# Kernel optimization log

Hardware: AMD Instinct MI355X
Metric: run time of the kernel (lower is better)

Reference implementation:

```python
import jax, jax.numpy as jnp
import numpy as np

LBDA = 0.5  # soft-min temperature, matches OTAM_cum_dist_v2 default


def setup_inputs() -> dict:
    key = jax.random.key(0)
    # frame distance scores (e.g. 1 - cosine similarity), in [0, 2]
    dists = jax.random.uniform(key, (200, 200, 32, 32), dtype=jnp.float32) * 2.0
    return {"dists": dists}


def _otam_cum_dist(dists, lbda=LBDA):
    """Faithful translation of OTAM_cum_dist_v2.

    dists: [Q, S, L, M] -> returns cum_dists[:, :, -1, -1] of shape [Q, S].
    The torch code pads the last dim by (1,1) with zeros, does a cumulative
    sum along row 0, and for each subsequent row a serial soft-min
    (-lbda * log(sum(exp(-x/lbda)))) recurrence along columns. Column 0 is
    never written and stays 0. Columns m==1 and m==Mp-1 include an extra
    diagonal/above term prev_row[m]; interior columns use only prev_row[m-1]
    and the running value cum[l, m-1].
    """
    Q, S, L, M = dists.shape
    Mp = M + 2
    # pad last dim by one zero on each side, move (L, Mp) to the front
    d = jnp.pad(dists, ((0, 0), (0, 0), (0, 0), (1, 1)))
    d = jnp.transpose(d, (2, 3, 0, 1))  # [L, Mp, Q, S]

    # row 0: cum[0, m] = cum[0, m-1] + d[0, m]; d[0,0]=0 so plain cumsum works
    row0 = jnp.cumsum(d[0], axis=0)  # [Mp, Q, S]

    m_idx = jnp.arange(1, Mp)
    mask3 = (m_idx == 1) | (m_idx == Mp - 1)  # columns with the 3-term soft-min

    def row_step(prev_row, d_row):
        # prev_row, d_row: [Mp, Q, S]
        def col_step(c, xs):
            d_m, p_m1, p_m, m3 = xs
            # soft-min: -lbda * log( exp(-p_m1/l) + exp(-c/l) [+ exp(-p_m/l)] )
            s = jnp.logaddexp(-p_m1 / lbda, -c / lbda)
            s = jnp.where(m3, jnp.logaddexp(s, -p_m / lbda), s)
            v = d_m - lbda * s
            return v, v

        xs = (d_row[1:], prev_row[:-1], prev_row[1:], mask3)
        _, vals = jax.lax.scan(col_step, jnp.zeros_like(d_row[0]), xs)
        new_row = jnp.concatenate([jnp.zeros_like(vals[:1]), vals], axis=0)
        return new_row, 0.0

    last_row, _ = jax.lax.scan(row_step, row0, d[1:])
    return last_row[-1]  # cum_dists[:, :, -1, -1] -> [Q, S]


def reference(dists):
    return _otam_cum_dist(dists, LBDA)
```

## Files before the change

kernel.cpp:

```cpp
#include <hip/hip_runtime.h>
#include <math.h>


constexpr int QS = 200 * 200;
constexpr int L = 32;
constexpr int M = 32;

__global__ __launch_bounds__(64) void otam_kernel(const float* __restrict__ dists,
                                                  float* __restrict__ out) {
    int p = blockIdx.x * blockDim.x + threadIdx.x;
    if (p >= QS) return;
    const float* dp = dists + (size_t)p * (L * M);

    float prev[34];
    float rowbuf[32];

    {
        const float4* r4 = (const float4*)dp;
#pragma unroll
        for (int i = 0; i < 8; ++i) {
            float4 v = r4[i];
            rowbuf[4 * i + 0] = v.x;
            rowbuf[4 * i + 1] = v.y;
            rowbuf[4 * i + 2] = v.z;
            rowbuf[4 * i + 3] = v.w;
        }
        float acc = 0.f;
        prev[0] = 0.f;
#pragma unroll
        for (int m = 1; m <= 32; ++m) {
            acc += rowbuf[m - 1];
            prev[m] = acc;
        }
        prev[33] = acc;
    }

    for (int l = 1; l < 32; ++l) {
        const float4* r4 = (const float4*)(dp + l * M);
#pragma unroll
        for (int i = 0; i < 8; ++i) {
            float4 v = r4[i];
            rowbuf[4 * i + 0] = v.x;
            rowbuf[4 * i + 1] = v.y;
            rowbuf[4 * i + 2] = v.z;
            rowbuf[4 * i + 3] = v.w;
        }
        float c = 0.f;
        float left = prev[0];
#pragma unroll
        for (int m = 1; m <= 33; ++m) {
            float dm = (m <= 32) ? rowbuf[m - 1] : 0.f;
            float pm1 = left;
            float pm = prev[m];
            bool m3 = (m == 1) || (m == 33);
            float mn = fminf(pm1, c);
            if (m3) mn = fminf(mn, pm);
            float sum = __expf(-2.f * (pm1 - mn)) + __expf(-2.f * (c - mn));
            if (m3) sum += __expf(-2.f * (pm - mn));
            float v = dm + mn - 0.5f * __logf(sum);
            left = prev[m];
            prev[m] = v;
            c = v;
        }
    }

    out[p] = prev[33];
}

extern "C" void kernel_launch(void* const* d_in, const int* in_sizes, int n_in,
                              void* d_out, int out_size, void* d_ws, size_t ws_size,
                              hipStream_t stream) {
    const float* dists = (const float*)d_in[0];
    float* out = (float*)d_out;
    dim3 grid((QS + 63) / 64);
    dim3 block(64);
    hipLaunchKernelGGL(otam_kernel, grid, block, 0, stream, dists, out);
}
```

Before: 264.4 us.

## Parallelize OTAM DP as anti-diagonal wavefront with one lane per row

```diff
diff --git a/kernel.cpp b/kernel.cpp
--- a/kernel.cpp
+++ b/kernel.cpp
@@ -2,69 +2,58 @@
 #include <math.h>
 
 
-constexpr int QS = 200 * 200;
-constexpr int L = 32;
-constexpr int M = 32;
+constexpr int QS = 40000;
+constexpr int PPB = 8;
 
-__global__ __launch_bounds__(64) void otam_kernel(const float* __restrict__ dists,
-                                                  float* __restrict__ out) {
-    int p = blockIdx.x * blockDim.x + threadIdx.x;
-    if (p >= QS) return;
-    const float* dp = dists + (size_t)p * (L * M);
-
-    float prev[34];
-    float rowbuf[32];
+__global__ __launch_bounds__(256) void otam_wavefront(const float* __restrict__ dists,
+                                                      float* __restrict__ out) {
+    __shared__ float lds[PPB * 1024];
+    const int tid = threadIdx.x;
+    const int blockP0 = blockIdx.x * PPB;
 
     {
-        const float4* r4 = (const float4*)dp;
+        const float4* src = (const float4*)(dists + (size_t)blockP0 * 1024);
+        float4* dst = (float4*)lds;
 #pragma unroll
-        for (int i = 0; i < 8; ++i) {
-            float4 v = r4[i];
-            rowbuf[4 * i + 0] = v.x;
-            rowbuf[4 * i + 1] = v.y;
-            rowbuf[4 * i + 2] = v.z;
-            rowbuf[4 * i + 3] = v.w;
+        for (int i = 0; i < 8; ++i)
+            dst[tid + 256 * i] = src[tid + 256 * i];
+    }
+    __syncthreads();
+
+    const int lane = tid & 63;
+    const int sub  = lane >> 5;
+    const int l    = lane & 31;
+    const int pl   = (tid >> 6) * 2 + sub;
+    const float* dp = lds + pl * 1024 + l * 32;
+
+    float myval = 0.f;
+    float pm1   = 0.f;
+
+#pragma unroll 4
+    for (int t = 1; t <= 64; ++t) {
+        float pm = __shfl_up(myval, 1, 32);
+        int m = t - l;
+        int mi = m - 1;
+        mi = mi < 0 ? 0 : (mi > 31 ? 31 : mi);
+        float dm = (m >= 1 && m <= 32) ? dp[mi] : 0.f;
+
+        float nv;
+        if (l == 0) {
+            nv = myval + dm;
+        } else {
+            bool m3 = (m == 1) || (m == 33);
+            float mn = fminf(pm1, myval);
+            mn = m3 ? fminf(mn, pm) : mn;
+            float s = __expf(-2.f * (pm1 - mn)) + __expf(-2.f * (myval - mn));
+            s += m3 ? __expf(-2.f * (pm - mn)) : 0.f;
+            nv = dm + mn - 0.5f * __logf(s);
         }
-        float acc = 0.f;
-        prev[0] = 0.f;
-#pragma unroll
-        for (int m = 1; m <= 32; ++m) {
-            acc += rowbuf[m - 1];
-            prev[m] = acc;
-        }
-        prev[33] = acc;
+        bool active = (m >= 1) && (m <= 33);
+        myval = active ? nv : myval;
+        pm1 = pm;
     }
 
-    for (int l = 1; l < 32; ++l) {
-        const float4* r4 = (const float4*)(dp + l * M);
-#pragma unroll
-        for (int i = 0; i < 8; ++i) {
-            float4 v = r4[i];
-            rowbuf[4 * i + 0] = v.x;
-            rowbuf[4 * i + 1] = v.y;
-            rowbuf[4 * i + 2] = v.z;
-            rowbuf[4 * i + 3] = v.w;
-        }
-        float c = 0.f;
-        float left = prev[0];
-#pragma unroll
-        for (int m = 1; m <= 33; ++m) {
-            float dm = (m <= 32) ? rowbuf[m - 1] : 0.f;
-            float pm1 = left;
-            float pm = prev[m];
-            bool m3 = (m == 1) || (m == 33);
-            float mn = fminf(pm1, c);
-            if (m3) mn = fminf(mn, pm);
-            float sum = __expf(-2.f * (pm1 - mn)) + __expf(-2.f * (c - mn));
-            if (m3) sum += __expf(-2.f * (pm - mn));
-            float v = dm + mn - 0.5f * __logf(sum);
-            left = prev[m];
-            prev[m] = v;
-            c = v;
-        }
-    }
-
-    out[p] = prev[33];
+    if (l == 31) out[blockP0 + pl] = myval;
 }
 
 extern "C" void kernel_launch(void* const* d_in, const int* in_sizes, int n_in,
@@ -72,7 +61,7 @@
                               hipStream_t stream) {
     const float* dists = (const float*)d_in[0];
     float* out = (float*)d_out;
-    dim3 grid((QS + 63) / 64);
-    dim3 block(64);
-    hipLaunchKernelGGL(otam_kernel, grid, block, 0, stream, dists, out);
+    dim3 grid(QS / PPB);
+    dim3 block(256);
+    hipLaunchKernelGGL(otam_wavefront, grid, block, 0, stream, dists, out);
 }
```

Result: faster. 253.1 us (-4.3%).

## Rewrite soft-min as log1p-of-difference with raw exp2/log and prefetch next row

Applied to the files above, without the earlier changes.

```diff
diff --git a/kernel.cpp b/kernel.cpp
--- a/kernel.cpp
+++ b/kernel.cpp
@@ -1,67 +1,74 @@
 #include <hip/hip_runtime.h>
-#include <math.h>
 
 
-constexpr int QS = 200 * 200;
-constexpr int L = 32;
-constexpr int M = 32;
+constexpr int QS = 40000;
 
-__global__ __launch_bounds__(64) void otam_kernel(const float* __restrict__ dists,
+__global__ __launch_bounds__(64, 1) void otam_tpp(const float* __restrict__ dists,
                                                   float* __restrict__ out) {
-    int p = blockIdx.x * blockDim.x + threadIdx.x;
-    if (p >= QS) return;
-    const float* dp = dists + (size_t)p * (L * M);
+    const int p = blockIdx.x * 64 + threadIdx.x;
+    const float* dp = dists + (size_t)p * 1024;
+
+    const float K = -2.8853900817779268f;
+    const float C2 = -0.34657359027997264f;
+
+    auto sm2 = [&](float a, float b) {
+        float mn = fminf(a, b);
+        float e = __builtin_amdgcn_exp2f(K * __builtin_fabsf(a - b));
+        return fmaf(C2, __builtin_amdgcn_logf(1.f + e), mn);
+    };
 
     float prev[34];
-    float rowbuf[32];
 
     {
+        float4 b[8];
         const float4* r4 = (const float4*)dp;
 #pragma unroll
-        for (int i = 0; i < 8; ++i) {
-            float4 v = r4[i];
-            rowbuf[4 * i + 0] = v.x;
-            rowbuf[4 * i + 1] = v.y;
-            rowbuf[4 * i + 2] = v.z;
-            rowbuf[4 * i + 3] = v.w;
-        }
+        for (int i = 0; i < 8; ++i) b[i] = r4[i];
         float acc = 0.f;
         prev[0] = 0.f;
 #pragma unroll
-        for (int m = 1; m <= 32; ++m) {
-            acc += rowbuf[m - 1];
-            prev[m] = acc;
+        for (int i = 0; i < 8; ++i) {
+            acc += b[i].x; prev[4 * i + 1] = acc;
+            acc += b[i].y; prev[4 * i + 2] = acc;
+            acc += b[i].z; prev[4 * i + 3] = acc;
+            acc += b[i].w; prev[4 * i + 4] = acc;
         }
         prev[33] = acc;
     }
 
+    float4 buf[8];
+    {
+        const float4* r4 = (const float4*)(dp + 32);
+#pragma unroll
+        for (int i = 0; i < 8; ++i) buf[i] = r4[i];
+    }
+
+#pragma unroll 2
     for (int l = 1; l < 32; ++l) {
-        const float4* r4 = (const float4*)(dp + l * M);
+        float4 nbuf[8];
+        if (l < 31) {
+            const float4* r4 = (const float4*)(dp + (l + 1) * 32);
 #pragma unroll
-        for (int i = 0; i < 8; ++i) {
-            float4 v = r4[i];
-            rowbuf[4 * i + 0] = v.x;
-            rowbuf[4 * i + 1] = v.y;
-            rowbuf[4 * i + 2] = v.z;
-            rowbuf[4 * i + 3] = v.w;
+            for (int i = 0; i < 8; ++i) nbuf[i] = r4[i];
         }
-        float c = 0.f;
-        float left = prev[0];
+        const float* dr = (const float*)buf;
+
+        float np[34];
+        np[0] = 0.f;
+        float c = dr[0] + sm2(C2, prev[1]);
+        np[1] = c;
 #pragma unroll
-        for (int m = 1; m <= 33; ++m) {
-            float dm = (m <= 32) ? rowbuf[m - 1] : 0.f;
-            float pm1 = left;
-            float pm = prev[m];
-            bool m3 = (m == 1) || (m == 33);
-            float mn = fminf(pm1, c);
-            if (m3) mn = fminf(mn, pm);
-            float sum = __expf(-2.f * (pm1 - mn)) + __expf(-2.f * (c - mn));
-            if (m3) sum += __expf(-2.f * (pm - mn));
-            float v = dm + mn - 0.5f * __logf(sum);
-            left = prev[m];
-            prev[m] = v;
-            c = v;
+        for (int m = 2; m <= 32; ++m) {
+            c = dr[m - 1] + sm2(prev[m - 1], c);
+            np[m] = c;
         }
+        c = sm2(sm2(prev[32], c), prev[33]);
+        np[33] = c;
+
+#pragma unroll
+        for (int i = 0; i < 34; ++i) prev[i] = np[i];
+#pragma unroll
+        for (int i = 0; i < 8; ++i) buf[i] = nbuf[i];
     }
 
     out[p] = prev[33];
@@ -72,7 +79,7 @@
                               hipStream_t stream) {
     const float* dists = (const float*)d_in[0];
     float* out = (float*)d_out;
-    dim3 grid((QS + 63) / 64);
+    dim3 grid(QS / 64);
     dim3 block(64);
-    hipLaunchKernelGGL(otam_kernel, grid, block, 0, stream, dists, out);
+    hipLaunchKernelGGL(otam_tpp, grid, block, 0, stream, dists, out);
 }
```

New measurement: 235.5 us. 1.12x faster.
